# Kernel tuning notes

Measured on AMD Instinct MI355X. Metric: run time of the kernel, lower is better.

Reference implementation:

```python
import jax, jax.numpy as jnp
import numpy as np

B, IN, H, OUT, BS = 2048, 1024, 2048, 1024, 32
RB = H // BS   # 64 block rows of fc2
CB = H // BS   # 64 block cols of fc2
DENSITY = 0.5
K = int(CB * DENSITY)  # 32 nonzero block-cols per block row
NNZ = RB * K           # 2048 nonzero blocks


def setup_inputs() -> dict:
    key = jax.random.key(0)
    k0, k1, k2, k3, k4, k5, k6 = jax.random.split(key, 7)
    # Fixed BSR sparsity structure (constant indices), built with numpy
    rng = np.random.default_rng(0)
    cols = np.stack([np.sort(rng.choice(CB, size=K, replace=False)) for _ in range(RB)])
    col_indices = jnp.asarray(cols.reshape(-1), dtype=jnp.int32)          # [NNZ]
    crow_indices = jnp.asarray(np.arange(RB + 1) * K, dtype=jnp.int32)    # [RB+1]
    s = 0.02
    return {
        "x": jax.random.normal(k0, (B, IN), jnp.float32),
        "W1": jax.random.normal(k1, (H, IN), jnp.float32) * s,
        "b1": jax.random.normal(k2, (H,), jnp.float32) * s,
        "crow_indices": crow_indices,
        "col_indices": col_indices,
        "values": jax.random.normal(k3, (NNZ, BS, BS), jnp.float32) * s,  # BSR blocks of fc2.weight [H,H]
        "b2": jax.random.normal(k4, (H,), jnp.float32) * s,
        "W3": jax.random.normal(k5, (OUT, H), jnp.float32) * s,
        "b3": jax.random.normal(k6, (OUT,), jnp.float32) * s,
    }


def bsr_linear(h, crow_indices, col_indices, values, bias):
    # y = h @ W.T + bias, W stored as BSR (block rows = out blocks, block cols = in blocks)
    b = h.shape[0]
    nnz, bs, _ = values.shape
    rb = crow_indices.shape[0] - 1
    hb = h.reshape(b, -1, bs)                      # [B, CB, bs]
    hg = hb[:, col_indices]                        # [B, NNZ, bs] gather input blocks per nnz block
    # contribution of block k (row r, col c): x_block[c] @ values[k].T
    contrib = jnp.einsum("bnj,nij->nbi", hg, values)  # [NNZ, B, bs]
    # block-row id of each nnz block, jit-safe via searchsorted on crow
    row_ids = jnp.searchsorted(crow_indices, jnp.arange(nnz, dtype=crow_indices.dtype), side="right") - 1
    yb = jax.ops.segment_sum(contrib, row_ids, num_segments=rb)  # [RB, B, bs]
    return jnp.transpose(yb, (1, 0, 2)).reshape(b, rb * bs) + bias


def reference(x, W1, b1, crow_indices, col_indices, values, b2, W3, b3):
    x = x.reshape(x.shape[0], -1)                 # Flatten
    h = jax.nn.relu(x @ W1.T + b1)                # fc1 + ReLU
    h = jax.nn.relu(bsr_linear(h, crow_indices, col_indices, values, b2))  # BSR fc2 + ReLU
    return h @ W3.T + b3                          # fc3
```

## Files before the change

### kernel.cpp

```cpp
#include <hip/hip_runtime.h>
#include <hip/hip_bf16.h>


typedef __attribute__((ext_vector_type(8))) short bf16x8;
typedef __attribute__((ext_vector_type(4))) float f32x4;

__device__ __forceinline__ unsigned short f2bf(float f) {
    union { float f; unsigned int u; } c; c.f = f;
    unsigned int u = c.u;
    u += 0x7fffu + ((u >> 16) & 1u);
    return (unsigned short)(u >> 16);
}

__device__ __forceinline__ void async16(const void* g, void* l) {
    __builtin_amdgcn_global_load_lds(
        (const __attribute__((address_space(1))) void*)g,
        (__attribute__((address_space(3))) void*)l,
        16, 0, 0);
}

__global__ __launch_bounds__(256) void cvt4(
    const float* __restrict__ x,  const float* __restrict__ w1,
    const float* __restrict__ w3, const float* __restrict__ v,
    unsigned short* __restrict__ xb,  unsigned short* __restrict__ w1b,
    unsigned short* __restrict__ w3b, unsigned short* __restrict__ vb)
{
    const int NE = 1 << 21;
    int e = (blockIdx.x * 256 + threadIdx.x) * 4;
    int a = e >> 21;
    int off = e & (NE - 1);
    const float* src = (a == 0) ? x : (a == 1) ? w1 : (a == 2) ? w3 : v;
    unsigned short* dst = (a == 0) ? xb : (a == 1) ? w1b : (a == 2) ? w3b : vb;
    float4 vv = *reinterpret_cast<const float4*>(src + off);
    ushort4 o;
    o.x = f2bf(vv.x); o.y = f2bf(vv.y); o.z = f2bf(vv.z); o.w = f2bf(vv.w);
    *reinterpret_cast<ushort4*>(dst + off) = o;
}

template<int BM, int BN, int MCL, int RELU, int OUT_BF16>
__global__ __launch_bounds__(256) void gemm_bt(
    const unsigned short* __restrict__ A,
    const unsigned short* __restrict__ B,
    const float* __restrict__ bias,
    void* __restrict__ Cout,
    int M, int N, int K)
{
    constexpr int BK = 64;
    constexpr int MR = BM / 32;
    constexpr int NR = BN / 32;
    constexpr int AI = BM / 32;
    constexpr int BI = BN / 32;
    __shared__ unsigned short As[2][BM * BK];
    __shared__ unsigned short Bs[2][BN * BK];

    const int t = threadIdx.x;
    const int w = t >> 6;
    const int l = t & 63;

    const int id = blockIdx.x;
    const int xcd = id & 7;
    const int j = id >> 3;
    const int mt = xcd * MCL + (j & (MCL - 1));
    const int nt = j / MCL;
    const int bm = mt * BM;
    const int bn = nt * BN;

    const int wm = (w >> 1) * (BM / 2);
    const int wn = (w & 1) * (BN / 2);

    f32x4 acc[MR][NR];
    #pragma unroll
    for (int i = 0; i < MR; ++i)
        #pragma unroll
        for (int jj = 0; jj < NR; ++jj)
            acc[i][jj] = (f32x4){0.f, 0.f, 0.f, 0.f};

    const int arow = bm + w * (BM / 4) + (l >> 3);
    const int brow = bn + w * (BN / 4) + (l >> 3);
    const int scol = ((l & 7) ^ (l >> 3)) * 8;

    const int fr = l & 15;
    const int kg = l >> 4;
    const int fq = l >> 4;

    auto stage = [&](int buf, int kt) {
        const int k0 = kt * BK;
        #pragma unroll
        for (int i = 0; i < AI; ++i)
            async16(A + (size_t)(arow + i * 8) * K + k0 + scol,
                    &As[buf][(w * (BM / 4) + i * 8) * BK]);
        #pragma unroll
        for (int i = 0; i < BI; ++i)
            async16(B + (size_t)(brow + i * 8) * K + k0 + scol,
                    &Bs[buf][(w * (BN / 4) + i * 8) * BK]);
    };

    auto compute = [&](int buf) {
        #pragma unroll
        for (int kk = 0; kk < 2; ++kk) {
            const int pc = ((kk * 4 + kg) ^ (fr & 7)) * 8;
            bf16x8 af[MR], bg[NR];
            #pragma unroll
            for (int i = 0; i < MR; ++i)
                af[i] = *reinterpret_cast<const bf16x8*>(
                    &As[buf][(wm + i * 16 + fr) * BK + pc]);
            #pragma unroll
            for (int jj = 0; jj < NR; ++jj)
                bg[jj] = *reinterpret_cast<const bf16x8*>(
                    &Bs[buf][(wn + jj * 16 + fr) * BK + pc]);
            #pragma unroll
            for (int i = 0; i < MR; ++i)
                #pragma unroll
                for (int jj = 0; jj < NR; ++jj)
                    acc[i][jj] = __builtin_amdgcn_mfma_f32_16x16x32_bf16(
                        af[i], bg[jj], acc[i][jj], 0, 0, 0);
        }
    };

    const int nK = K >> 6;
    int cur = 0;
    stage(0, 0);
    __syncthreads();
    for (int kt = 0; kt < nK - 1; ++kt) {
        stage(cur ^ 1, kt + 1);
        compute(cur);
        __syncthreads();
        cur ^= 1;
    }
    compute(cur);

    #pragma unroll
    for (int i = 0; i < MR; ++i) {
        const int row0 = bm + wm + i * 16 + fq * 4;
        #pragma unroll
        for (int jj = 0; jj < NR; ++jj) {
            const int col = bn + wn + jj * 16 + fr;
            const float bv = bias[col];
            #pragma unroll
            for (int v = 0; v < 4; ++v) {
                float r = acc[i][jj][v] + bv;
                if (RELU) r = fmaxf(r, 0.f);
                const size_t off = (size_t)(row0 + v) * N + col;
                if (OUT_BF16) ((unsigned short*)Cout)[off] = f2bf(r);
                else          ((float*)Cout)[off] = r;
            }
        }
    }
}

__global__ __launch_bounds__(256) void bsr_layer(
    const unsigned short* __restrict__ h,
    const int* __restrict__ crow,
    const int* __restrict__ cols,
    const unsigned short* __restrict__ vals,
    const float* __restrict__ b2,
    unsigned short* __restrict__ h2)
{
    __shared__ unsigned short Hs[2][128 * 64];
    __shared__ unsigned short Vs[2][32 * 64];
    __shared__ int colsS[64];
    const int t = threadIdx.x;
    const int w = t >> 6;
    const int l = t & 63;

    const int id = blockIdx.x;
    const int xcd = id & 7;
    const int j2 = id >> 3;
    const int bt = xcd * 2 + (j2 & 1);
    const int r  = j2 >> 1;
    const int bm = bt * 128;

    const int s = crow[r];
    const int cnt = crow[r + 1] - s;
    const int wrow = w * 32;

    if (t < cnt) colsS[t] = cols[s + t];

    f32x4 acc[2][2];
    #pragma unroll
    for (int i = 0; i < 2; ++i)
        #pragma unroll
        for (int jj = 0; jj < 2; ++jj)
            acc[i][jj] = (f32x4){0.f, 0.f, 0.f, 0.f};

    const int fr = l & 15;
    const int kg = l >> 4;
    const int lr = l >> 3;
    const int sc = (l & 7) ^ lr;

    auto stage = [&](int buf, int js) {
        const int n0 = s + 2 * js;
        const bool tail = (2 * js + 1 >= cnt);
        const int c0 = colsS[2 * js];
        const int c1 = tail ? c0 : colsS[2 * js + 1];
        const int n1 = tail ? n0 : n0 + 1;
        #pragma unroll
        for (int i = 0; i < 4; ++i) {
            const int row = bm + w * 32 + i * 8 + lr;
            const int col = (sc & 4) ? c1 * 32 + (sc & 3) * 8 : c0 * 32 + sc * 8;
            async16(h + (size_t)row * 2048 + col,
                    &Hs[buf][(w * 32 + i * 8) * 64]);
        }
        const int vrow = w * 8 + lr;
        if (!tail || !(sc & 4)) {
            const unsigned short* src =
                vals + (size_t)((sc & 4) ? n1 : n0) * 1024 + vrow * 32 + (sc & 3) * 8;
            async16(src, &Vs[buf][(w * 8) * 64]);
        } else {
            bf16x8 z = (bf16x8){0,0,0,0,0,0,0,0};
            *reinterpret_cast<bf16x8*>(&Vs[buf][vrow * 64 + (l & 7) * 8]) = z;
        }
    };

    auto compute = [&](int buf) {
        #pragma unroll
        for (int kk = 0; kk < 2; ++kk) {
            const int pc = ((kk * 4 + kg) ^ (fr & 7)) * 8;
            bf16x8 af[2], bg[2];
            #pragma unroll
            for (int i = 0; i < 2; ++i)
                af[i] = *reinterpret_cast<const bf16x8*>(
                    &Hs[buf][(wrow + i * 16 + fr) * 64 + pc]);
            #pragma unroll
            for (int jj = 0; jj < 2; ++jj)
                bg[jj] = *reinterpret_cast<const bf16x8*>(
                    &Vs[buf][(jj * 16 + fr) * 64 + pc]);
            #pragma unroll
            for (int i = 0; i < 2; ++i)
                #pragma unroll
                for (int jj = 0; jj < 2; ++jj)
                    acc[i][jj] = __builtin_amdgcn_mfma_f32_16x16x32_bf16(
                        af[i], bg[jj], acc[i][jj], 0, 0, 0);
        }
    };

    __syncthreads();
    const int nsteps = (cnt + 1) >> 1;
    int cur = 0;
    stage(0, 0);
    __syncthreads();
    for (int js = 0; js < nsteps - 1; ++js) {
        stage(cur ^ 1, js + 1);
        compute(cur);
        __syncthreads();
        cur ^= 1;
    }
    compute(cur);

    const int fq = l >> 4;
    #pragma unroll
    for (int i = 0; i < 2; ++i) {
        const int row0 = bm + wrow + i * 16 + fq * 4;
        #pragma unroll
        for (int jj = 0; jj < 2; ++jj) {
            const int col = r * 32 + jj * 16 + fr;
            const float bv = b2[col];
            #pragma unroll
            for (int v = 0; v < 4; ++v) {
                float rv = fmaxf(acc[i][jj][v] + bv, 0.f);
                h2[(size_t)(row0 + v) * 2048 + col] = f2bf(rv);
            }
        }
    }
}

extern "C" void kernel_launch(void* const* d_in, const int* in_sizes, int n_in,
                              void* d_out, int out_size, void* d_ws, size_t ws_size,
                              hipStream_t stream) {
    const float* x    = (const float*)d_in[0];
    const float* W1   = (const float*)d_in[1];
    const float* b1   = (const float*)d_in[2];
    const int*   crow = (const int*)d_in[3];
    const int*   cols = (const int*)d_in[4];
    const float* vals = (const float*)d_in[5];
    const float* b2   = (const float*)d_in[6];
    const float* W3   = (const float*)d_in[7];
    const float* b3   = (const float*)d_in[8];
    float* out = (float*)d_out;

    const int NE = 2 * 1024 * 1024;
    unsigned short* xb  = (unsigned short*)d_ws;
    unsigned short* w1b = xb  + NE;
    unsigned short* w3b = w1b + NE;
    unsigned short* vb  = w3b + NE;
    unsigned short* hb  = vb  + NE;
    unsigned short* h2b = hb  + 2 * NE;

    cvt4<<<8192, 256, 0, stream>>>(x, W1, W3, vals, xb, w1b, w3b, vb);

    gemm_bt<128, 64, 2, 1, 1><<<512, 256, 0, stream>>>(
        xb, w1b, b1, hb, 2048, 2048, 1024);
    bsr_layer<<<1024, 256, 0, stream>>>(hb, crow, cols, vb, b2, h2b);
    gemm_bt<64, 64, 4, 0, 0><<<512, 256, 0, stream>>>(
        h2b, w3b, b3, out, 2048, 1024, 2048);

    (void)in_sizes; (void)n_in; (void)out_size; (void)ws_size;
}
```

Measured before the change: 84.25 us.

## Prefetch two stages ahead with explicit vmcnt waits in GEMM and BSR kernels

Restructures the double-buffered main loops of the dense GEMM and the BSR fc2 kernel so two tiles are in flight. Each step waits only on the older group's loads via s_waitcnt vmcnt, then uses raw barriers, replacing __syncthreads, which drains all outstanding loads. This is meant to hide global-to-LDS latency behind MFMA work. It relies on exact per-thread load counts (LPS, 5) matching what stage() issues. If those counts are wrong, a race occurs.

```diff
diff --git a/kernel.cpp b/kernel.cpp
--- a/kernel.cpp
+++ b/kernel.cpp
@@ -17,6 +17,16 @@
         (const __attribute__((address_space(1))) void*)g,
         (__attribute__((address_space(3))) void*)l,
         16, 0, 0);
+}
+
+template<int N>
+__device__ __forceinline__ void vm_wait() {
+    asm volatile("s_waitcnt vmcnt(%0)" :: "n"(N) : "memory");
+}
+__device__ __forceinline__ void barrier() {
+    asm volatile("" ::: "memory");
+    __builtin_amdgcn_s_barrier();
+    asm volatile("" ::: "memory");
 }
 
 __global__ __launch_bounds__(256) void cvt4(
@@ -50,6 +60,7 @@
     constexpr int NR = BN / 32;
     constexpr int AI = BM / 32;
     constexpr int BI = BN / 32;
+    constexpr int LPS = AI + BI;
     __shared__ unsigned short As[2][BM * BK];
     __shared__ unsigned short Bs[2][BN * BK];
 
@@ -118,15 +129,19 @@
     };
 
     const int nK = K >> 6;
+    stage(0, 0);
+    stage(1, 1);
     int cur = 0;
-    stage(0, 0);
-    __syncthreads();
     for (int kt = 0; kt < nK - 1; ++kt) {
-        stage(cur ^ 1, kt + 1);
+        vm_wait<LPS>();
+        barrier();
         compute(cur);
-        __syncthreads();
+        barrier();
+        if (kt + 2 < nK) stage(cur, kt + 2);
         cur ^= 1;
     }
+    vm_wait<0>();
+    barrier();
     compute(cur);
 
     #pragma unroll
@@ -236,15 +251,19 @@
 
     __syncthreads();
     const int nsteps = (cnt + 1) >> 1;
+    stage(0, 0);
+    if (nsteps > 1) stage(1, 1);
     int cur = 0;
-    stage(0, 0);
-    __syncthreads();
     for (int js = 0; js < nsteps - 1; ++js) {
-        stage(cur ^ 1, js + 1);
+        vm_wait<5>();
+        barrier();
         compute(cur);
-        __syncthreads();
+        barrier();
+        if (js + 2 < nsteps) stage(cur, js + 2);
         cur ^= 1;
     }
+    vm_wait<0>();
+    barrier();
     compute(cur);
 
     const int fq = l >> 4;
```

Result: faster. 79.58 us (-5.5%).
